# Performance work log

Hardware: AMD Instinct MI355X
Metric: run time of the kernel (lower is better)

The kernel has to match this reference:

```python
import jax, jax.numpy as jnp
import numpy as np

B, F_, J, D = 64, 256, 25, 3
FILT = 64
N = B * F_ * J
EPS = 1e-5


def setup_inputs() -> dict:
    key = jax.random.key(0)
    ks = jax.random.split(key, 20)
    x = jax.random.normal(ks[0], (B, F_, J, D), jnp.float32)
    # block-diagonal skeleton: chain bones, bidirectional, tiled over B*F graphs
    bones = np.stack([np.arange(J - 1), np.arange(1, J)], axis=1)  # (24,2)
    e = np.concatenate([bones, bones[:, ::-1]], axis=0)            # (48,2)
    G = B * F_
    off = (np.arange(G, dtype=np.int64) * J)[:, None, None]
    edge_index = jnp.asarray((e[None].astype(np.int64) + off).reshape(-1, 2).T)  # (2, G*48)
    s = 0.1
    W1 = jax.random.normal(ks[1], (D, FILT), jnp.float32) * s
    b1 = jnp.zeros((FILT,), jnp.float32)
    g1 = jnp.ones((FILT,), jnp.float32)
    be1 = jnp.zeros((FILT,), jnp.float32)
    W2 = jax.random.normal(ks[2], (FILT, FILT), jnp.float32) * s
    b2 = jnp.zeros((FILT,), jnp.float32)
    g2 = jnp.ones((FILT,), jnp.float32)
    be2 = jnp.zeros((FILT,), jnp.float32)
    cw1 = jax.random.normal(ks[3], (2 * FILT, J * FILT, 3), jnp.float32) * 0.02  # OIH
    cb1 = jnp.zeros((2 * FILT,), jnp.float32)
    cg1 = jnp.ones((2 * FILT,), jnp.float32)
    cbe1 = jnp.zeros((2 * FILT,), jnp.float32)
    cw2 = jax.random.normal(ks[4], (FILT, 2 * FILT, 1), jnp.float32) * 0.05
    cb2 = jnp.zeros((FILT,), jnp.float32)
    cg2 = jnp.ones((FILT,), jnp.float32)
    cbe2 = jnp.zeros((FILT,), jnp.float32)
    return dict(x=x, edge_index=edge_index, batch_size=B, frame_l=F_,
                W1=W1, b1=b1, g1=g1, be1=be1, W2=W2, b2=b2, g2=g2, be2=be2,
                cw1=cw1, cb1=cb1, cg1=cg1, cbe1=cbe1,
                cw2=cw2, cb2=cb2, cg2=cg2, cbe2=cbe2)


def _lrelu(v):
    return jnp.where(v >= 0, v, 0.2 * v)


def _bn_nodes(v, g, b):  # BatchNorm1d on (N, C), batch stats
    m = v.mean(0)
    var = v.var(0)
    return g * (v - m) * jax.lax.rsqrt(var + EPS) + b


def _bn_ncl(v, g, b):  # BatchNorm1d on (B, C, L), batch stats
    m = v.mean((0, 2), keepdims=True)
    var = v.var((0, 2), keepdims=True)
    return g[None, :, None] * (v - m) * jax.lax.rsqrt(var + EPS) + b[None, :, None]


def _gcn(h_in, W, b, src, dst, n):
    # PyG GCNConv: h' = D^{-1/2} (A+I) D^{-1/2} h W + b
    h = h_in @ W
    loop = jnp.arange(n, dtype=src.dtype)
    sa = jnp.concatenate([src, loop])
    da = jnp.concatenate([dst, loop])
    deg = jax.ops.segment_sum(jnp.ones(sa.shape[0], h.dtype), da, num_segments=n)
    dinv = jnp.where(deg > 0, jax.lax.rsqrt(deg), 0.0)
    norm = dinv[sa] * dinv[da]
    return jax.ops.segment_sum(h[sa] * norm[:, None], da, num_segments=n) + b


def _conv1d(v, w, pad):  # v:(B,C,L), w:(O,I,K)
    return jax.lax.conv_general_dilated(v, w, window_strides=(1,), padding=((pad, pad),),
                                         dimension_numbers=("NCH", "OIH", "NCH"))


def reference(x, edge_index, batch_size, frame_l, W1, b1, g1, be1, W2, b2, g2, be2,
              cw1, cb1, cg1, cbe1, cw2, cb2, cg2, cbe2):
    src, dst = edge_index[0], edge_index[1]
    n = x.shape[0] * x.shape[1] * x.shape[2]
    h = x.reshape(-1, x.shape[-1])                               # (N, D)
    h = _lrelu(_bn_nodes(_gcn(h, W1, b1, src, dst, n), g1, be1))  # (N, FILT)
    h = _lrelu(_bn_nodes(_gcn(h, W2, b2, src, dst, n), g2, be2))  # (N, FILT)
    t = h.reshape(batch_size, frame_l, -1).transpose(0, 2, 1)     # (B, J*FILT, L)
    t = _lrelu(_bn_ncl(_conv1d(t, cw1, 1) + cb1[None, :, None], cg1, cbe1))  # dropout: eval = identity
    t = _lrelu(_bn_ncl(_conv1d(t, cw2, 0) + cb2[None, :, None], cg2, cbe2))
    return t.transpose(0, 2, 1)                                   # (B, L, FILT)
```

## Files before the change

### kernel.cpp

```cpp
#include <hip/hip_runtime.h>
#include <stdint.h>

#define B_ 64
#define F2_ 256
#define J_ 25
#define FILT_ 64
#define C1_ 1600
#define O1_ 128
#define NN_ 409600
#define MM_ 16384
#define EPSV 1e-5f

typedef short short8 __attribute__((ext_vector_type(8)));
typedef float f32x4 __attribute__((ext_vector_type(4)));

static const size_t WS_Y2T  = 0;
static const size_t WS_XA   = 52838400;
static const size_t WS_WT1  = 57753600;
static const size_t WS_WT2  = 58982400;
static const size_t WS_WT2G = 58998784;
static const size_t WS_Y3   = 59006976;
static const size_t WS_Y4   = 67395584;
static const size_t WS_ST   = 71589888;
#define ST_S9    0
#define ST_SUM2  16
#define ST_SQ2   80
#define ST_SUM3  144
#define ST_SQ3   272
#define ST_SUM4  400
#define ST_SQ4   464
#define ST_S1    528
#define ST_T1    592
#define ST_SC2   656
#define ST_SH2   720
#define ST_SC3   784
#define ST_SH3   912
#define ST_SC4   1040
#define ST_SH4   1104
#define ST_COUNT 1168

__device__ __forceinline__ float bf2f(unsigned int u){
  return __uint_as_float(u << 16);
}
__device__ __forceinline__ unsigned short f2bf(float f){
  unsigned int u = __float_as_uint(f);
  u += 0x7fffu + ((u >> 16) & 1u);
  return (unsigned short)(u >> 16);
}
__device__ __forceinline__ float lrelu(float x){ return fmaxf(x, 0.2f * x); }
__device__ __forceinline__ float wsum(float v){
  #pragma unroll
  for (int off = 32; off > 0; off >>= 1) v += __shfl_down(v, off, 64);
  return v;
}

typedef __attribute__((address_space(3))) unsigned int lds_uint_t;
typedef __attribute__((address_space(1))) const unsigned int glob_uint_t;
__device__ __forceinline__ void gl16(const void* g, void* l){
  __builtin_amdgcn_global_load_lds((glob_uint_t*)g, (lds_uint_t*)l, 16, 0, 0);
}

__global__ __launch_bounds__(256) void k_zpad(unsigned short* __restrict__ y2j){
  int b = blockIdx.x, tid = threadIdx.x;
  for (int i = tid; i < 400; i += 256){
    int j = i >> 4;
    int r = (i >> 3) & 1;
    int s = i & 7;
    uint4* p = (uint4*)(y2j + ((size_t)(b * 25 + j) * 258 + (r ? 257 : 0)) * 64) + s;
    *p = make_uint4(0, 0, 0, 0);
  }
}

__global__ __launch_bounds__(256) void k_wt(const float* __restrict__ cw1,
                                            const float* __restrict__ W2,
                                            const float* __restrict__ cw2,
                                            unsigned short* __restrict__ wt1,
                                            unsigned short* __restrict__ wt2,
                                            unsigned short* __restrict__ wt2g){
  int blk = blockIdx.x;
  if (blk < 384){
    int k = blk >> 7, o = blk & 127;
    for (int c = threadIdx.x; c < 1600; c += 256)
      wt1[(size_t)(k * 128 + o) * 1600 + c] = f2bf(cw1[(size_t)(o * 1600 + c) * 3 + k]);
  } else if (blk < 416){
    int idx = ((blk - 384) << 8) + threadIdx.x;
    wt2[idx] = f2bf(cw2[idx]);
  } else {
    int idx = ((blk - 416) << 8) + threadIdx.x;
    int f = idx >> 6, cc = idx & 63;
    wt2g[idx] = f2bf(W2[cc * 64 + f]);
  }
}

__global__ __launch_bounds__(256) void k_gcn1(const float* __restrict__ x,
                                              float* __restrict__ xa,
                                              float* __restrict__ S9){
  int n = blockIdx.x * 256 + threadIdx.x;
  int j = n % J_;
  float dj  = (j == 0 || j == J_-1) ? 2.f : 3.f;
  float rdj = rsqrtf(dj);
  const float* xp = x + (size_t)n * 3;
  float wg = 1.f / dj;
  float a0 = xp[0]*wg, a1 = xp[1]*wg, a2 = xp[2]*wg;
  if (j > 0){
    float dm = (j == 1) ? 2.f : 3.f;  float w = rdj * rsqrtf(dm);
    a0 += xp[-3]*w; a1 += xp[-2]*w; a2 += xp[-1]*w;
  }
  if (j < J_-1){
    float dp = (j == J_-2) ? 2.f : 3.f;  float w = rdj * rsqrtf(dp);
    a0 += xp[3]*w; a1 += xp[4]*w; a2 += xp[5]*w;
  }
  float* xo = xa + (size_t)n * 3;
  xo[0] = a0; xo[1] = a1; xo[2] = a2;
  float p[9] = {a0, a1, a2, a0*a0, a0*a1, a0*a2, a1*a1, a1*a2, a2*a2};
  __shared__ float tmp[9][4];
  int wv = threadIdx.x >> 6, ln = threadIdx.x & 63;
  #pragma unroll
  for (int k = 0; k < 9; k++){ float s = wsum(p[k]); if (ln == 0) tmp[k][wv] = s; }
  __syncthreads();
  if (threadIdx.x < 9){
    int k = threadIdx.x;
    atomicAdd(S9 + k, tmp[k][0] + tmp[k][1] + tmp[k][2] + tmp[k][3]);
  }
}

__global__ void k_bn1(const float* __restrict__ S9, const float* __restrict__ W1,
                      const float* __restrict__ b1, const float* __restrict__ g1,
                      const float* __restrict__ be1,
                      float* __restrict__ s1, float* __restrict__ t1){
  int c = threadIdx.x;
  float inv = 1.f / (float)NN_;
  float m0 = S9[0]*inv, m1 = S9[1]*inv, m2 = S9[2]*inv;
  float C00 = S9[3]*inv - m0*m0, C01 = S9[4]*inv - m0*m1, C02 = S9[5]*inv - m0*m2;
  float C11 = S9[6]*inv - m1*m1, C12 = S9[7]*inv - m1*m2, C22 = S9[8]*inv - m2*m2;
  float w0 = W1[c], w1 = W1[64+c], w2 = W1[128+c];
  float mean = m0*w0 + m1*w1 + m2*w2 + b1[c];
  float var  = w0*w0*C00 + w1*w1*C11 + w2*w2*C22
             + 2.f*(w0*w1*C01 + w0*w2*C02 + w1*w2*C12);
  float s = g1[c] * rsqrtf(var + EPSV);
  s1[c] = s;
  t1[c] = be1[c] - s*mean + s*b1[c];
}

#define H1SLICE(ph, js) do { \
  int js_ = (js); \
  _Pragma("unroll") \
  for (int i_ = 0; i_ < 16; i_++){ \
    const float* xp_ = xas + ((size_t)(wl0 + i_) * 25 + js_) * 3; \
    h[ph][i_] = lrelu(fmaf(sS, fmaf(xp_[0], w0c, fmaf(xp_[1], w1c, xp_[2]*w2c)), tT)); \
  } } while(0)

#define AGGW(pm, pc, pp) do { \
  _Pragma("unroll") \
  for (int i_ = 0; i_ < 16; i_++){ \
    float a_ = wgm*h[pm][i_] + wgs*h[pc][i_] + wgp*h[pp][i_]; \
    *(unsigned short*)(Ab + i_*128 + ((((lane>>3)) ^ (i_&7))<<4) + ((lane&7)<<1)) = f2bf(a_); \
  } } while(0)

__global__ __launch_bounds__(256) void k_gcn2m(const float* __restrict__ xa,
                                               const float* __restrict__ W1,
                                               const float* __restrict__ s1,
                                               const float* __restrict__ t1,
                                               const float* __restrict__ b2,
                                               const unsigned short* __restrict__ wt2g,
                                               unsigned short* __restrict__ y2j,
                                               float* __restrict__ sum2,
                                               float* __restrict__ sq2){
  __shared__ float xas[4800];
  __shared__ float prm[384];
  __shared__ char Bs[8192];
  __shared__ char Aw[4][2048];
  __shared__ char Cw[4][2048];
  int blk = blockIdx.x;
  int jh = blk & 1;
  int lq = (blk >> 1) & 3;
  int b  = blk >> 3;
  int l0 = lq << 6;
  int tid = threadIdx.x;
  int w = tid >> 6, lane = tid & 63;

  const float* xsrc = xa + (size_t)(b * 256 + l0) * 75;
  #pragma unroll
  for (int i = 0; i < 5; i++){
    int idx = tid + (i << 8);
    if (idx < 1200) ((float4*)xas)[idx] = ((const float4*)xsrc)[idx];
  }
  prm[tid] = (tid < 192) ? W1[tid] : s1[tid - 192];
  if (tid < 128) prm[256 + tid] = (tid < 64) ? t1[tid] : b2[tid - 64];
  #pragma unroll
  for (int i = 0; i < 2; i++){
    int r = (w << 4) + (i << 3) + (lane >> 3);
    int cblk = lane & 7;
    gl16(wt2g + (size_t)r * 64 + (((cblk ^ (r & 7))) << 3),
         Bs + (w << 11) + (i << 10));
  }
  __syncthreads();

  int kgl = lane >> 4;
  short8 bf[2][4];
  #pragma unroll
  for (int ks = 0; ks < 2; ks++){
    #pragma unroll
    for (int nf = 0; nf < 4; nf++){
      int row = (nf << 4) + (lane & 15);
      int kb = kgl + (ks << 2);
      bf[ks][nf] = *(const short8*)(Bs + (row << 7) + ((kb ^ (row & 7)) << 4));
    }
  }
  float w0c = prm[lane], w1c = prm[64 + lane], w2c = prm[128 + lane];
  float sS = prm[192 + lane], tT = prm[256 + lane];
  float bias[4];
  #pragma unroll
  for (int nf = 0; nf < 4; nf++) bias[nf] = prm[320 + (nf << 4) + (lane & 15)];
  int wl0 = w << 4;
  char* Ab = Aw[w];
  char* Cb = Cw[w];

  float h[3][16];
  int J0 = jh ? 12 : 0;
  int NJ = jh ? 13 : 12;
  #pragma unroll
  for (int i = 0; i < 16; i++) h[2][i] = 0.f;
  H1SLICE(0, J0);
  if (J0 > 0) H1SLICE(2, J0 - 1);

  float ss[4] = {0,0,0,0}, qq[4] = {0,0,0,0};

  #pragma unroll
  for (int jj = 0; jj < 13; jj++){
    if (jj >= NJ) break;
    int j = J0 + jj;
    if (j + 1 <= 24){
      switch ((jj + 1) % 3){
        case 0: H1SLICE(0, j + 1); break;
        case 1: H1SLICE(1, j + 1); break;
        case 2: H1SLICE(2, j + 1); break;
      }
    }
    float dj  = (j == 0 || j == 24) ? 2.f : 3.f;
    float rdj = rsqrtf(dj);
    float wgs = 1.f / dj;
    float wgm = (j > 0)  ? rdj * rsqrtf((j == 1)  ? 2.f : 3.f) : 0.f;
    float wgp = (j < 24) ? rdj * rsqrtf((j == 23) ? 2.f : 3.f) : 0.f;
    switch (jj % 3){
      case 0: AGGW(2, 0, 1); break;
      case 1: AGGW(0, 1, 2); break;
      case 2: AGGW(1, 2, 0); break;
    }
    f32x4 acc[4] = {};
    #pragma unroll
    for (int ks = 0; ks < 2; ks++){
      int kb = kgl + (ks << 2);
      int m0w = lane & 15;
      short8 a = *(const short8*)(Ab + (m0w << 7) + ((kb ^ (m0w & 7)) << 4));
      acc[0] = __builtin_amdgcn_mfma_f32_16x16x32_bf16(a, bf[ks][0], acc[0], 0, 0, 0);
      acc[1] = __builtin_amdgcn_mfma_f32_16x16x32_bf16(a, bf[ks][1], acc[1], 0, 0, 0);
      acc[2] = __builtin_amdgcn_mfma_f32_16x16x32_bf16(a, bf[ks][2], acc[2], 0, 0, 0);
      acc[3] = __builtin_amdgcn_mfma_f32_16x16x32_bf16(a, bf[ks][3], acc[3], 0, 0, 0);
    }
    int rowb = kgl << 2;
    int col15 = lane & 15;
    #pragma unroll
    for (int nf = 0; nf < 4; nf++){
      #pragma unroll
      for (int r = 0; r < 4; r++){
        float v = acc[nf][r] + bias[nf];
        ss[nf] += v; qq[nf] += v * v;
        int row = rowb + r;
        *(unsigned short*)(Cb + row * 128 +
            ((nf ^ ((row >> 2) & 3)) << 5) + (col15 << 1)) = f2bf(v);
      }
    }
    unsigned short* dst = y2j + ((size_t)(b * 25 + j) * 258 + l0 + wl0 + 1) * 64;
    #pragma unroll
    for (int it = 0; it < 2; it++){
      int idx = lane + (it << 6);
      int row = idx >> 3, slot = idx & 7;
      uint4 u = *(const uint4*)(Cb + row * 128 +
                ((((slot >> 1) ^ ((row >> 2) & 3)) << 5) + ((slot & 1) << 4)));
      *(uint4*)(dst + row * 64 + (slot << 3)) = u;
    }
  }
  #pragma unroll
  for (int nf = 0; nf < 4; nf++){
    ss[nf] += __shfl_xor(ss[nf], 16, 64); ss[nf] += __shfl_xor(ss[nf], 32, 64);
    qq[nf] += __shfl_xor(qq[nf], 16, 64); qq[nf] += __shfl_xor(qq[nf], 32, 64);
  }
  if (lane < 16){
    #pragma unroll
    for (int nf = 0; nf < 4; nf++){
      atomicAdd(sum2 + (nf << 4) + lane, ss[nf]);
      atomicAdd(sq2  + (nf << 4) + lane, qq[nf]);
    }
  }
}

__global__ void k_bnp(const float* __restrict__ sum, const float* __restrict__ sq,
                      const float* __restrict__ g, const float* __restrict__ be,
                      float* __restrict__ sc, float* __restrict__ sh, float inv){
  int c = threadIdx.x;
  float mean = sum[c] * inv;
  float var  = sq[c] * inv - mean * mean;
  float s = g[c] * rsqrtf(var + EPSV);
  sc[c] = s; sh[c] = be[c] - s * mean;
}

__global__ __launch_bounds__(256) void k_bnapp2(unsigned short* __restrict__ y2j,
                                                const float* __restrict__ sc2,
                                                const float* __restrict__ sh2){
  for (unsigned idx = blockIdx.x * 256 + threadIdx.x; idx < 3276800u; idx += 524288u){
    unsigned bj = idx >> 11;
    unsigned rem = idx & 2047u;
    unsigned l = rem >> 3;
    unsigned slot = idx & 7u;
    uint4* p = (uint4*)y2j + ((size_t)bj * 258 + l + 1) * 8 + slot;
    unsigned f0 = slot << 3;
    float4 sa = *(const float4*)(sc2 + f0);
    float4 sb = *(const float4*)(sc2 + f0 + 4);
    float4 ha = *(const float4*)(sh2 + f0);
    float4 hb = *(const float4*)(sh2 + f0 + 4);
    float scs[8] = {sa.x,sa.y,sa.z,sa.w,sb.x,sb.y,sb.z,sb.w};
    float shs[8] = {ha.x,ha.y,ha.z,ha.w,hb.x,hb.y,hb.z,hb.w};
    uint4 v = *p;
    unsigned vv[4] = {v.x,v.y,v.z,v.w};
    unsigned r[4];
    #pragma unroll
    for (int i = 0; i < 4; i++){
      float lo = bf2f(vv[i] & 0xffffu);
      float hi = bf2f(vv[i] >> 16);
      lo = lrelu(fmaf(scs[2*i],   lo, shs[2*i]));
      hi = lrelu(fmaf(scs[2*i+1], hi, shs[2*i+1]));
      r[i] = (unsigned)f2bf(lo) | (((unsigned)f2bf(hi)) << 16);
    }
    *p = make_uint4(r[0],r[1],r[2],r[3]);
  }
}

#define NT_ 75
__global__ __launch_bounds__(256) void k_conv1(const unsigned short* __restrict__ y2j,
                                               const unsigned short* __restrict__ wt1,
                                               const float* __restrict__ cb1,
                                               float* __restrict__ y3,
                                               float* __restrict__ sum3,
                                               float* __restrict__ sq3){
  __shared__ char smem[32768];
  int bid = blockIdx.x;
  int blk = ((bid & 7) << 6) | (bid >> 3);
  int b  = blk >> 3;
  int lq = (blk >> 1) & 3;
  int og = blk & 1;
  int l0 = lq << 6;
  int tid = threadIdx.x;
  int w = tid >> 6, lane = tid & 63;
  int wm = w >> 1, wn = w & 1;
  const unsigned short* y2b = y2j + (size_t)b * 412800;
  const unsigned short* wtb = wt1 + (size_t)og * 64 * 1600;

  int rs = (w << 4) + (lane >> 3);
  int cblk = lane & 7;
  int m0 = (wm << 5) + (lane & 15);
  int n0 = (wn << 5) + (lane & 15);
  int kg = lane >> 4;

  f32x4 acc[2][2] = {};

  auto stage = [&](int t, int buf){
    int cc6 = (t * 0x5556) >> 16;
    int k   = t - cc6 * 3;
    int cc  = cc6 << 6;
    const unsigned short* wk = wtb + (size_t)k * 204800;
    #pragma unroll
    for (int i = 0; i < 2; i++){
      int r = rs + (i << 3);
      int sw = (cblk ^ (r & 7)) << 3;
      gl16(y2b + ((size_t)cc6 * 258 + l0 + r + k) * 64 + sw,
           smem + buf * 16384 + (w << 11) + (i << 10));
      gl16(wk + (size_t)r * 1600 + cc + sw,
           smem + buf * 16384 + 8192 + (w << 11) + (i << 10));
    }
  };

  stage(0, 0);
  __syncthreads();
  #pragma unroll 2
  for (int t = 0; t < NT_; ++t){
    int buf = t & 1;
    if (t + 1 < NT_) stage(t + 1, buf ^ 1);
    const char* Ab = smem + buf * 16384;
    const char* Bb = Ab + 8192;
    #pragma unroll
    for (int ks = 0; ks < 2; ks++){
      int kb = kg + (ks << 2);
      short8 a0 = *(const short8*)(Ab + (m0 << 7)        + ((kb ^ (m0 & 7)) << 4));
      short8 a1 = *(const short8*)(Ab + ((m0 + 16) << 7) + ((kb ^ (m0 & 7)) << 4));
      short8 b0 = *(const short8*)(Bb + (n0 << 7)        + ((kb ^ (n0 & 7)) << 4));
      short8 b1 = *(const short8*)(Bb + ((n0 + 16) << 7) + ((kb ^ (n0 & 7)) << 4));
      acc[0][0] = __builtin_amdgcn_mfma_f32_16x16x32_bf16(a0, b0, acc[0][0], 0, 0, 0);
      acc[0][1] = __builtin_amdgcn_mfma_f32_16x16x32_bf16(a0, b1, acc[0][1], 0, 0, 0);
      acc[1][0] = __builtin_amdgcn_mfma_f32_16x16x32_bf16(a1, b0, acc[1][0], 0, 0, 0);
      acc[1][1] = __builtin_amdgcn_mfma_f32_16x16x32_bf16(a1, b1, acc[1][1], 0, 0, 0);
    }
    __syncthreads();
  }

  int colb = (og << 6) + n0;
  int rowb = l0 + (wm << 5) + ((lane >> 4) << 2);
  float ss0 = 0.f, ss1 = 0.f, qq0 = 0.f, qq1 = 0.f;
  #pragma unroll
  for (int mi = 0; mi < 2; mi++){
    #pragma unroll
    for (int ni = 0; ni < 2; ni++){
      int col = colb + (ni << 4);
      float bias = cb1[col];
      #pragma unroll
      for (int r = 0; r < 4; r++){
        float v = acc[mi][ni][r] + bias;
        if (ni){ ss1 += v; qq1 += v * v; } else { ss0 += v; qq0 += v * v; }
        y3[(size_t)((b << 8) + rowb + (mi << 4) + r) * 128 + col] = v;
      }
    }
  }
  ss0 += __shfl_xor(ss0, 16, 64); ss0 += __shfl_xor(ss0, 32, 64);
  ss1 += __shfl_xor(ss1, 16, 64); ss1 += __shfl_xor(ss1, 32, 64);
  qq0 += __shfl_xor(qq0, 16, 64); qq0 += __shfl_xor(qq0, 32, 64);
  qq1 += __shfl_xor(qq1, 16, 64); qq1 += __shfl_xor(qq1, 32, 64);
  if ((lane >> 4) == 0){
    atomicAdd(sum3 + colb, ss0);      atomicAdd(sq3 + colb, qq0);
    atomicAdd(sum3 + colb + 16, ss1); atomicAdd(sq3 + colb + 16, qq1);
  }
}

__global__ __launch_bounds__(256) void k_conv2(const float* __restrict__ y3,
                                               const float* __restrict__ sc3,
                                               const float* __restrict__ sh3,
                                               const unsigned short* __restrict__ wt2,
                                               const float* __restrict__ cb2,
                                               float* __restrict__ y4,
                                               float* __restrict__ sum4,
                                               float* __restrict__ sq4){
  __shared__ char smem[32768];
  int blk = blockIdx.x;
  int b = blk >> 2, lq = blk & 3;
  int l0 = lq << 6;
  int tid = threadIdx.x;
  int w = tid >> 6, lane = tid & 63;
  int wm = w >> 1, wn = w & 1;
  #pragma unroll
  for (int i = 0; i < 4; i++){
    int r = (w << 4) + (i << 2) + (lane >> 4);
    int sw = (((lane & 15) ^ (r & 7)) << 3);
    gl16(wt2 + (size_t)r * 128 + sw, smem + 16384 + (w << 12) + (i << 10));
  }
  #pragma unroll
  for (int i = 0; i < 4; i++){
    int idx = tid + (i << 8);
    int r = idx >> 4, s = idx & 15;
    const float* src = y3 + (size_t)((b << 8) + l0 + r) * 128 + (s << 3);
    float4 v0 = *(const float4*)(src);
    float4 v1 = *(const float4*)(src + 4);
    float4 c0 = *(const float4*)(sc3 + (s << 3));
    float4 c1 = *(const float4*)(sc3 + (s << 3) + 4);
    float4 h0 = *(const float4*)(sh3 + (s << 3));
    float4 h1 = *(const float4*)(sh3 + (s << 3) + 4);
    uint4 u;
    u.x = (unsigned)f2bf(lrelu(fmaf(c0.x, v0.x, h0.x))) |
          ((unsigned)f2bf(lrelu(fmaf(c0.y, v0.y, h0.y))) << 16);
    u.y = (unsigned)f2bf(lrelu(fmaf(c0.z, v0.z, h0.z))) |
          ((unsigned)f2bf(lrelu(fmaf(c0.w, v0.w, h0.w))) << 16);
    u.z = (unsigned)f2bf(lrelu(fmaf(c1.x, v1.x, h1.x))) |
          ((unsigned)f2bf(lrelu(fmaf(c1.y, v1.y, h1.y))) << 16);
    u.w = (unsigned)f2bf(lrelu(fmaf(c1.z, v1.z, h1.z))) |
          ((unsigned)f2bf(lrelu(fmaf(c1.w, v1.w, h1.w))) << 16);
    *(uint4*)(smem + r * 256 + ((s ^ (r & 7)) << 4)) = u;
  }
  __syncthreads();
  f32x4 acc[2][2] = {};
  int m0 = (wm << 5) + (lane & 15);
  int n0 = (wn << 5) + (lane & 15);
  int kg = lane >> 4;
  const char* Ab = smem;
  const char* Bb = smem + 16384;
  #pragma unroll
  for (int ks = 0; ks < 4; ks++){
    int kb = kg + (ks << 2);
    short8 a0 = *(const short8*)(Ab + (m0 << 8)        + ((kb ^ (m0 & 7)) << 4));
    short8 a1 = *(const short8*)(Ab + ((m0 + 16) << 8) + ((kb ^ (m0 & 7)) << 4));
    short8 b0 = *(const short8*)(Bb + (n0 << 8)        + ((kb ^ (n0 & 7)) << 4));
    short8 b1 = *(const short8*)(Bb + ((n0 + 16) << 8) + ((kb ^ (n0 & 7)) << 4));
    acc[0][0] = __builtin_amdgcn_mfma_f32_16x16x32_bf16(a0, b0, acc[0][0], 0, 0, 0);
    acc[0][1] = __builtin_amdgcn_mfma_f32_16x16x32_bf16(a0, b1, acc[0][1], 0, 0, 0);
    acc[1][0] = __builtin_amdgcn_mfma_f32_16x16x32_bf16(a1, b0, acc[1][0], 0, 0, 0);
    acc[1][1] = __builtin_amdgcn_mfma_f32_16x16x32_bf16(a1, b1, acc[1][1], 0, 0, 0);
  }
  int rowb = l0 + (wm << 5) + ((lane >> 4) << 2);
  float ss0 = 0.f, ss1 = 0.f, qq0 = 0.f, qq1 = 0.f;
  #pragma unroll
  for (int mi = 0; mi < 2; mi++){
    #pragma unroll
    for (int ni = 0; ni < 2; ni++){
      int f = n0 + (ni << 4);
      float bias = cb2[f];
      #pragma unroll
      for (int r = 0; r < 4; r++){
        float v = acc[mi][ni][r] + bias;
        if (ni){ ss1 += v; qq1 += v * v; } else { ss0 += v; qq0 += v * v; }
        y4[(size_t)((b << 8) + rowb + (mi << 4) + r) * 64 + f] = v;
      }
    }
  }
  ss0 += __shfl_xor(ss0, 16, 64); ss0 += __shfl_xor(ss0, 32, 64);
  ss1 += __shfl_xor(ss1, 16, 64); ss1 += __shfl_xor(ss1, 32, 64);
  qq0 += __shfl_xor(qq0, 16, 64); qq0 += __shfl_xor(qq0, 32, 64);
  qq1 += __shfl_xor(qq1, 16, 64); qq1 += __shfl_xor(qq1, 32, 64);
  if ((lane >> 4) == 0){
    atomicAdd(sum4 + n0, ss0);      atomicAdd(sq4 + n0, qq0);
    atomicAdd(sum4 + n0 + 16, ss1); atomicAdd(sq4 + n0 + 16, qq1);
  }
}

__global__ __launch_bounds__(256) void k_final(const float* __restrict__ y4,
                                               const float* __restrict__ sc4,
                                               const float* __restrict__ sh4,
                                               float* __restrict__ out){
  unsigned q = blockIdx.x * 256 + threadIdx.x;
  unsigned f0 = (q & 15) << 2;
  float4 v = ((const float4*)y4)[q];
  float4 sc = *(const float4*)(sc4 + f0);
  float4 sh = *(const float4*)(sh4 + f0);
  v.x = lrelu(fmaf(sc.x, v.x, sh.x));
  v.y = lrelu(fmaf(sc.y, v.y, sh.y));
  v.z = lrelu(fmaf(sc.z, v.z, sh.z));
  v.w = lrelu(fmaf(sc.w, v.w, sh.w));
  ((float4*)out)[q] = v;
}

extern "C" void kernel_launch(void* const* d_in, const int* in_sizes, int n_in,
                              void* d_out, int out_size, void* d_ws, size_t ws_size,
                              hipStream_t stream){
  const float* x    = (const float*)d_in[0];
  const float* W1   = (const float*)d_in[4];
  const float* b1   = (const float*)d_in[5];
  const float* g1   = (const float*)d_in[6];
  const float* be1  = (const float*)d_in[7];
  const float* W2   = (const float*)d_in[8];
  const float* b2   = (const float*)d_in[9];
  const float* g2   = (const float*)d_in[10];
  const float* be2  = (const float*)d_in[11];
  const float* cw1  = (const float*)d_in[12];
  const float* cb1  = (const float*)d_in[13];
  const float* cg1  = (const float*)d_in[14];
  const float* cbe1 = (const float*)d_in[15];
  const float* cw2  = (const float*)d_in[16];
  const float* cb2  = (const float*)d_in[17];
  const float* cg2  = (const float*)d_in[18];
  const float* cbe2 = (const float*)d_in[19];

  char* ws = (char*)d_ws;
  unsigned short* y2j  = (unsigned short*)(ws + WS_Y2T);
  float* xa            = (float*)(ws + WS_XA);
  unsigned short* wt1  = (unsigned short*)(ws + WS_WT1);
  unsigned short* wt2  = (unsigned short*)(ws + WS_WT2);
  unsigned short* wt2g = (unsigned short*)(ws + WS_WT2G);
  float* y3            = (float*)(ws + WS_Y3);
  float* y4            = (float*)(ws + WS_Y4);
  float* st            = (float*)(ws + WS_ST);

  if (ws_size < WS_ST + ST_COUNT * 4) return;

  hipMemsetAsync(st, 0, ST_COUNT * 4, stream);
  k_zpad  <<<64, 256, 0, stream>>>(y2j);
  k_wt    <<<432, 256, 0, stream>>>(cw1, W2, cw2, wt1, wt2, wt2g);
  k_gcn1  <<<1600, 256, 0, stream>>>(x, xa, st + ST_S9);
  k_bn1   <<<1, 64, 0, stream>>>(st + ST_S9, W1, b1, g1, be1, st + ST_S1, st + ST_T1);
  k_gcn2m <<<512, 256, 0, stream>>>(xa, W1, st + ST_S1, st + ST_T1, b2, wt2g,
                                    y2j, st + ST_SUM2, st + ST_SQ2);
  k_bnp   <<<1, 64, 0, stream>>>(st + ST_SUM2, st + ST_SQ2, g2, be2,
                                 st + ST_SC2, st + ST_SH2, 1.f / (float)NN_);
  k_bnapp2<<<2048, 256, 0, stream>>>(y2j, st + ST_SC2, st + ST_SH2);
  k_conv1 <<<512, 256, 0, stream>>>(y2j, wt1, cb1, y3, st + ST_SUM3, st + ST_SQ3);
  k_bnp   <<<1, 128, 0, stream>>>(st + ST_SUM3, st + ST_SQ3, cg1, cbe1,
                                  st + ST_SC3, st + ST_SH3, 1.f / (float)MM_);
  k_conv2 <<<256, 256, 0, stream>>>(y3, st + ST_SC3, st + ST_SH3, wt2, cb2,
                                    y4, st + ST_SUM4, st + ST_SQ4);
  k_bnp   <<<1, 64, 0, stream>>>(st + ST_SUM4, st + ST_SQ4, cg2, cbe2,
                                 st + ST_SC4, st + ST_SH4, 1.f / (float)MM_);
  k_final <<<1024, 256, 0, stream>>>(y4, st + ST_SC4, st + ST_SH4, (float*)d_out);
}
```

Baseline: 202.5 us.

## Keep GCN2 tiles in registers and remove LDS staging from k_gcn2m

The GCN layer-2 kernel no longer stages x, parameters, weight tiles or A/C fragments in shared memory. Each lane now reads its own node row of x and its channel slice of the parameters straight from global memory, builds the MFMA A fragments in registers, and prefetches the next joint's inputs one step ahead. Output bf16 values are stored directly with scattered 2-byte writes instead of going through an LDS transpose followed by 16-byte stores. This removes the LDS traffic and the barrier, but costs more registers and gives less coalesced global loads and stores.

```diff
diff --git a/kernel.cpp b/kernel.cpp
--- a/kernel.cpp
+++ b/kernel.cpp
@@ -142,19 +142,16 @@
   t1[c] = be1[c] - s*mean + s*b1[c];
 }
 
-#define H1SLICE(ph, js) do { \
-  int js_ = (js); \
+#define HCOMP(ph, x0_, x1_, x2_) do { \
   _Pragma("unroll") \
   for (int i_ = 0; i_ < 16; i_++){ \
-    const float* xp_ = xas + ((size_t)(wl0 + i_) * 25 + js_) * 3; \
-    h[ph][i_] = lrelu(fmaf(sS, fmaf(xp_[0], w0c, fmaf(xp_[1], w1c, xp_[2]*w2c)), tT)); \
+    h[ph][i_] = lrelu(fmaf(sSc[i_], fmaf((x0_), w0c[i_], fmaf((x1_), w1cc[i_], (x2_)*w2c[i_])), tTc[i_])); \
   } } while(0)
 
-#define AGGW(pm, pc, pp) do { \
+#define AGGP(pm, pc, pp) do { \
   _Pragma("unroll") \
   for (int i_ = 0; i_ < 16; i_++){ \
-    float a_ = wgm*h[pm][i_] + wgs*h[pc][i_] + wgp*h[pp][i_]; \
-    *(unsigned short*)(Ab + i_*128 + ((((lane>>3)) ^ (i_&7))<<4) + ((lane&7)<<1)) = f2bf(a_); \
+    av[i_] = wgm*h[pm][i_] + wgs*h[pc][i_] + wgp*h[pp][i_]; \
   } } while(0)
 
 __global__ __launch_bounds__(256) void k_gcn2m(const float* __restrict__ xa,
@@ -166,11 +163,6 @@
                                                unsigned short* __restrict__ y2j,
                                                float* __restrict__ sum2,
                                                float* __restrict__ sq2){
-  __shared__ float xas[4800];
-  __shared__ float prm[384];
-  __shared__ char Bs[8192];
-  __shared__ char Aw[4][2048];
-  __shared__ char Cw[4][2048];
   int blk = blockIdx.x;
   int jh = blk & 1;
   int lq = (blk >> 1) & 3;
@@ -178,51 +170,45 @@
   int l0 = lq << 6;
   int tid = threadIdx.x;
   int w = tid >> 6, lane = tid & 63;
-
-  const float* xsrc = xa + (size_t)(b * 256 + l0) * 75;
-  #pragma unroll
-  for (int i = 0; i < 5; i++){
-    int idx = tid + (i << 8);
-    if (idx < 1200) ((float4*)xas)[idx] = ((const float4*)xsrc)[idx];
-  }
-  prm[tid] = (tid < 192) ? W1[tid] : s1[tid - 192];
-  if (tid < 128) prm[256 + tid] = (tid < 64) ? t1[tid] : b2[tid - 64];
-  #pragma unroll
-  for (int i = 0; i < 2; i++){
-    int r = (w << 4) + (i << 3) + (lane >> 3);
-    int cblk = lane & 7;
-    gl16(wt2g + (size_t)r * 64 + (((cblk ^ (r & 7))) << 3),
-         Bs + (w << 11) + (i << 10));
-  }
-  __syncthreads();
-
-  int kgl = lane >> 4;
+  int m = lane & 15, kg = lane >> 4;
+
+  const float* xrow = xa + (size_t)(b * 256 + l0 + (w << 4) + m) * 75;
+
+  float w0c[16], w1cc[16], w2c[16], sSc[16], tTc[16];
+  #pragma unroll
+  for (int i = 0; i < 16; i++){
+    int c = ((i >> 3) << 5) + (kg << 3) + (i & 7);
+    w0c[i] = W1[c]; w1cc[i] = W1[64 + c]; w2c[i] = W1[128 + c];
+    sSc[i] = s1[c]; tTc[i] = t1[c];
+  }
   short8 bf[2][4];
   #pragma unroll
   for (int ks = 0; ks < 2; ks++){
     #pragma unroll
     for (int nf = 0; nf < 4; nf++){
-      int row = (nf << 4) + (lane & 15);
-      int kb = kgl + (ks << 2);
-      bf[ks][nf] = *(const short8*)(Bs + (row << 7) + ((kb ^ (row & 7)) << 4));
-    }
-  }
-  float w0c = prm[lane], w1c = prm[64 + lane], w2c = prm[128 + lane];
-  float sS = prm[192 + lane], tT = prm[256 + lane];
+      bf[ks][nf] = *(const short8*)(wt2g + (size_t)((nf << 4) + m) * 64 + (ks << 5) + (kg << 3));
+    }
+  }
   float bias[4];
   #pragma unroll
-  for (int nf = 0; nf < 4; nf++) bias[nf] = prm[320 + (nf << 4) + (lane & 15)];
-  int wl0 = w << 4;
-  char* Ab = Aw[w];
-  char* Cb = Cw[w];
-
-  float h[3][16];
+  for (int nf = 0; nf < 4; nf++) bias[nf] = b2[(nf << 4) + m];
+
   int J0 = jh ? 12 : 0;
   int NJ = jh ? 13 : 12;
+
+  float h[3][16];
   #pragma unroll
   for (int i = 0; i < 16; i++) h[2][i] = 0.f;
-  H1SLICE(0, J0);
-  if (J0 > 0) H1SLICE(2, J0 - 1);
+  {
+    float x0 = xrow[J0*3], x1 = xrow[J0*3+1], x2 = xrow[J0*3+2];
+    HCOMP(0, x0, x1, x2);
+    float z0 = xrow[(J0+1)*3], z1 = xrow[(J0+1)*3+1], z2 = xrow[(J0+1)*3+2];
+    HCOMP(1, z0, z1, z2);
+    if (jh){
+      float y0 = xrow[33], y1 = xrow[34], y2v = xrow[35];
+      HCOMP(2, y0, y1, y2v);
+    }
+  }
 
   float ss[4] = {0,0,0,0}, qq[4] = {0,0,0,0};
 
@@ -230,55 +216,51 @@
   for (int jj = 0; jj < 13; jj++){
     if (jj >= NJ) break;
     int j = J0 + jj;
-    if (j + 1 <= 24){
-      switch ((jj + 1) % 3){
-        case 0: H1SLICE(0, j + 1); break;
-        case 1: H1SLICE(1, j + 1); break;
-        case 2: H1SLICE(2, j + 1); break;
-      }
+    float p0 = 0.f, p1 = 0.f, p2 = 0.f;
+    bool needp = (jj < NJ - 1) && (j + 2 <= 24);
+    if (needp){
+      p0 = xrow[(j+2)*3]; p1 = xrow[(j+2)*3+1]; p2 = xrow[(j+2)*3+2];
     }
     float dj  = (j == 0 || j == 24) ? 2.f : 3.f;
     float rdj = rsqrtf(dj);
     float wgs = 1.f / dj;
     float wgm = (j > 0)  ? rdj * rsqrtf((j == 1)  ? 2.f : 3.f) : 0.f;
     float wgp = (j < 24) ? rdj * rsqrtf((j == 23) ? 2.f : 3.f) : 0.f;
+    float av[16];
     switch (jj % 3){
-      case 0: AGGW(2, 0, 1); break;
-      case 1: AGGW(0, 1, 2); break;
-      case 2: AGGW(1, 2, 0); break;
+      case 0: AGGP(2, 0, 1); break;
+      case 1: AGGP(0, 1, 2); break;
+      case 2: AGGP(1, 2, 0); break;
+    }
+    short8 af0, af1;
+    #pragma unroll
+    for (int i = 0; i < 8; i++){
+      af0[i] = (short)f2bf(av[i]);
+      af1[i] = (short)f2bf(av[8 + i]);
     }
     f32x4 acc[4] = {};
     #pragma unroll
-    for (int ks = 0; ks < 2; ks++){
-      int kb = kgl + (ks << 2);
-      int m0w = lane & 15;
-      short8 a = *(const short8*)(Ab + (m0w << 7) + ((kb ^ (m0w & 7)) << 4));
-      acc[0] = __builtin_amdgcn_mfma_f32_16x16x32_bf16(a, bf[ks][0], acc[0], 0, 0, 0);
-      acc[1] = __builtin_amdgcn_mfma_f32_16x16x32_bf16(a, bf[ks][1], acc[1], 0, 0, 0);
-      acc[2] = __builtin_amdgcn_mfma_f32_16x16x32_bf16(a, bf[ks][2], acc[2], 0, 0, 0);
-      acc[3] = __builtin_amdgcn_mfma_f32_16x16x32_bf16(a, bf[ks][3], acc[3], 0, 0, 0);
-    }
-    int rowb = kgl << 2;
-    int col15 = lane & 15;
+    for (int nf = 0; nf < 4; nf++)
+      acc[nf] = __builtin_amdgcn_mfma_f32_16x16x32_bf16(af0, bf[0][nf], acc[nf], 0, 0, 0);
+    #pragma unroll
+    for (int nf = 0; nf < 4; nf++)
+      acc[nf] = __builtin_amdgcn_mfma_f32_16x16x32_bf16(af1, bf[1][nf], acc[nf], 0, 0, 0);
+    unsigned short* dst = y2j + ((size_t)(b * 25 + j) * 258 + l0 + (w << 4) + (kg << 2) + 1) * 64 + m;
     #pragma unroll
     for (int nf = 0; nf < 4; nf++){
       #pragma unroll
       for (int r = 0; r < 4; r++){
         float v = acc[nf][r] + bias[nf];
         ss[nf] += v; qq[nf] += v * v;
-        int row = rowb + r;
-        *(unsigned short*)(Cb + row * 128 +
-            ((nf ^ ((row >> 2) & 3)) << 5) + (col15 << 1)) = f2bf(v);
+        dst[(size_t)r * 64 + (nf << 4)] = f2bf(v);
       }
     }
-    unsigned short* dst = y2j + ((size_t)(b * 25 + j) * 258 + l0 + wl0 + 1) * 64;
-    #pragma unroll
-    for (int it = 0; it < 2; it++){
-      int idx = lane + (it << 6);
-      int row = idx >> 3, slot = idx & 7;
-      uint4 u = *(const uint4*)(Cb + row * 128 +
-                ((((slot >> 1) ^ ((row >> 2) & 3)) << 5) + ((slot & 1) << 4)));
-      *(uint4*)(dst + row * 64 + (slot << 3)) = u;
+    if (needp){
+      switch ((jj + 2) % 3){
+        case 0: HCOMP(0, p0, p1, p2); break;
+        case 1: HCOMP(1, p0, p1, p2); break;
+        case 2: HCOMP(2, p0, p1, p2); break;
+      }
     }
   }
   #pragma unroll
```

After: 196.7 us. 1.03x faster.
